# Optimization experiments

Hardware: AMD Instinct MI355X
Metric: run time of the kernel (lower is better)

## Reference

```python
import jax, jax.numpy as jnp
import numpy as np

H = 512

def setup_inputs() -> dict:
    key = jax.random.key(0)
    ks = jax.random.split(key, 10)
    T, B, S = 64, 8, 512
    scale = 1.0 / np.sqrt(H)
    return {
        "attn_dec_state": jax.random.normal(ks[0], (T, B, H), jnp.float32),
        "attn_enc_state": jax.random.normal(ks[1], (S, B, H), jnp.float32),
        "attn_coverage": jax.random.uniform(ks[2], (B, S), jnp.float32),
        "Wq": jax.random.normal(ks[3], (H, H), jnp.float32) * scale,   # linear_query weight (in,out)
        "bq": jnp.zeros((H,), jnp.float32),
        "Wc": jax.random.normal(ks[4], (H, H), jnp.float32) * scale,   # linear_context weight
        "v": jax.random.normal(ks[5], (H,), jnp.float32) * scale,       # v projection H->1
        "Wo": jax.random.normal(ks[6], (2 * H, H), jnp.float32) * scale,  # linear_out weight
        "bo": jnp.zeros((H,), jnp.float32),
        "wcov": jax.random.normal(ks[7], (H,), jnp.float32) * scale,    # linear_cover weight 1->H
    }

def reference(attn_dec_state, attn_enc_state, attn_coverage, Wq, bq, Wc, v, Wo, bo, wcov):
    dec = jnp.transpose(attn_dec_state, (1, 0, 2))   # [B,T,H]
    enc = jnp.transpose(attn_enc_state, (1, 0, 2))   # [B,S,H]
    # coverage: linear_cover(1->H) applied to each scalar, added to enc, then tanh
    enc = jnp.tanh(enc + attn_coverage[:, :, None] * wcov)  # [B,S,H]
    # additive (Bahdanau) score with broadcast-tanh
    a1 = jnp.einsum('bth,hk->btk', dec, Wq) + bq             # [B,T,H]
    a2 = jnp.einsum('bsh,hk->bsk', enc, Wc)                  # [B,S,H]
    scores = jnp.einsum('btsh,h->bts', jnp.tanh(a1[:, :, None, :] + a2[:, None, :, :]), v)  # [B,T,S]
    align = jax.nn.softmax(scores, axis=-1)                  # [B,T,S]
    c = jnp.einsum('bts,bsh->bth', align, enc)               # [B,T,H]
    concat = jnp.concatenate([c, dec], axis=-1)              # [B,T,2H]
    attn_h = jnp.einsum('btd,dk->btk', concat, Wo) + bo      # [B,T,H]
    attn_h = jnp.transpose(attn_h, (1, 0, 2))                # [T,B,H]
    align_out = jnp.transpose(align, (1, 0, 2))              # [T,B,S]
    return attn_h, align_out
```

## Files before the change

### kernel.cpp

```cpp
#include <hip/hip_runtime.h>
#include <cstddef>

static constexpr int TT = 64;
static constexpr int BB = 8;
static constexpr int SS = 512;
static constexpr int HH = 512;

typedef __attribute__((ext_vector_type(8))) short bf16x8;
typedef __attribute__((ext_vector_type(4))) float f32x4;

__device__ __forceinline__ float fast_tanh(float x) {
  float e = __expf(2.0f * x);
  return 1.0f - 2.0f * __builtin_amdgcn_rcpf(e + 1.0f);
}
__device__ __forceinline__ unsigned short f2bf(float f) {
  unsigned u = __float_as_uint(f);
  return (unsigned short)((u + 0x7FFFu + ((u >> 16) & 1u)) >> 16);
}

__global__ __launch_bounds__(256)
void k_prep(const float* __restrict__ enc, const float* __restrict__ cov,
            const float* __restrict__ wcov, const float* __restrict__ dec,
            const float* __restrict__ Wq, const float* __restrict__ Wc,
            const float* __restrict__ Wo,
            unsigned short* __restrict__ encpb, unsigned short* __restrict__ concatb,
            unsigned short* __restrict__ WqT, unsigned short* __restrict__ WcT,
            unsigned short* __restrict__ WoT) {
  __shared__ float tile[32][33];
  const int blk = blockIdx.x, tid = threadIdx.x;

  if (blk < 8192) {
    const int idx = blk * 256 + tid;
    const int h = idx & 511;
    const int bs = idx >> 9;
    const int s = bs & 511, b = bs >> 9;
    const float x = enc[(size_t)(s * BB + b) * HH + h] + cov[bs] * wcov[h];
    encpb[idx] = f2bf(fast_tanh(x));
  } else if (blk < 8704) {
    const int m = blk - 8192, t = m & 63, b = m >> 6;
    const float2 dv = *(const float2*)(dec + (size_t)(t * BB + b) * HH + 2 * tid);
    ((unsigned*)concatb)[(size_t)m * 512 + 256 + tid] =
        (unsigned)f2bf(dv.x) | ((unsigned)f2bf(dv.y) << 16);
  } else {
    int l = blk - 8704;
    const float* W; unsigned short* WT; int KT;
    if (l < 256)      { W = Wq; WT = WqT; KT = 512; }
    else if (l < 512) { W = Wc; WT = WcT; KT = 512; l -= 256; }
    else              { W = Wo; WT = WoT; KT = 1024; l -= 512; }
    const int n0 = (l & 15) * 32, k0 = (l >> 4) * 32;
    const int r = tid >> 3, c4 = (tid & 7) * 4;
    const float4 w = *(const float4*)(W + (size_t)(k0 + r) * 512 + n0 + c4);
    tile[r][c4 + 0] = w.x; tile[r][c4 + 1] = w.y;
    tile[r][c4 + 2] = w.z; tile[r][c4 + 3] = w.w;
    __syncthreads();
    unsigned short* o = WT + (size_t)(n0 + r) * KT + k0 + c4;
#pragma unroll
    for (int i = 0; i < 4; ++i) o[i] = f2bf(tile[c4 + i][r]);
  }
}

template<int LDA, int LDB>
__device__ __forceinline__ void gemm_tile(const unsigned short* __restrict__ A,
                                          const unsigned short* __restrict__ BT,
                                          int m0, int n0, int kbeg, int kend,
                                          unsigned short (*As)[72],
                                          unsigned short (*Bs)[72],
                                          f32x4 acc[4]) {
  const int tid = threadIdx.x, w = tid >> 6, lane = tid & 63;
  const int lr = tid >> 2, lk = (tid & 3) * 16;
  const int fm = w * 16 + (lane & 15), fk = (lane >> 4) * 8;
  for (int k0 = kbeg; k0 < kend; k0 += 64) {
    const uint4* ga = (const uint4*)(A + (size_t)(m0 + lr) * LDA + k0 + lk);
    const uint4* gb = (const uint4*)(BT + (size_t)(n0 + lr) * LDB + k0 + lk);
    uint4 a0 = ga[0], a1 = ga[1], b0 = gb[0], b1 = gb[1];
    *(uint4*)&As[lr][lk] = a0;  *(uint4*)&As[lr][lk + 8] = a1;
    *(uint4*)&Bs[lr][lk] = b0;  *(uint4*)&Bs[lr][lk + 8] = b1;
    __syncthreads();
#pragma unroll
    for (int ks = 0; ks < 2; ++ks) {
      bf16x8 af = *(const bf16x8*)&As[fm][ks * 32 + fk];
#pragma unroll
      for (int j = 0; j < 4; ++j) {
        bf16x8 bf = *(const bf16x8*)&Bs[j * 16 + (lane & 15)][ks * 32 + fk];
        acc[j] = __builtin_amdgcn_mfma_f32_16x16x32_bf16(af, bf, acc[j], 0, 0, 0);
      }
    }
    __syncthreads();
  }
}

__global__ __launch_bounds__(256)
void k_gemm12(const unsigned short* __restrict__ concatb,
              const unsigned short* __restrict__ encpb,
              const unsigned short* __restrict__ WqT,
              const unsigned short* __restrict__ WcT,
              const unsigned short* __restrict__ WoT,
              const float* __restrict__ bq, const float* __restrict__ bo,
              float* __restrict__ Ea1, float* __restrict__ Ea2,
              float* __restrict__ attn_h) {
  __shared__ unsigned short As[64][72];
  __shared__ unsigned short Bs[64][72];
  const int g = blockIdx.x, tid = threadIdx.x;
  const int w = tid >> 6, lane = tid & 63;
  const int col = lane & 15, rq = lane >> 4;

  if (g < 64) {
    const int m0 = (g >> 3) * 64, n0 = (g & 7) * 64;
    f32x4 acc[4] = {};
    gemm_tile<1024, 512>(concatb + 512, WqT, m0, n0, 0, 512, As, Bs, acc);
#pragma unroll
    for (int j = 0; j < 4; ++j) {
      const int n = n0 + j * 16 + col;
      const float bv = bq[n];
#pragma unroll
      for (int r = 0; r < 4; ++r) {
        const int m = m0 + w * 16 + rq * 4 + r;
        float val = fminf(fmaxf(acc[j][r] + bv, -30.0f), 30.0f);
        Ea1[(size_t)m * 512 + n] = __expf(2.0f * val);
      }
    }
  } else if (g < 576) {
    const int u = g - 64;
    const int m0 = (u >> 3) * 64, n0 = (u & 7) * 64;
    f32x4 acc[4] = {};
    gemm_tile<512, 512>(encpb, WcT, m0, n0, 0, 512, As, Bs, acc);
#pragma unroll
    for (int j = 0; j < 4; ++j) {
      const int n = n0 + j * 16 + col;
#pragma unroll
      for (int r = 0; r < 4; ++r) {
        const int m = m0 + w * 16 + rq * 4 + r;
        float val = fminf(fmaxf(acc[j][r], -30.0f), 30.0f);
        Ea2[(size_t)m * 512 + n] = __expf(2.0f * val);
      }
    }
  } else {
    const int u = g - 576;
    const int m0 = (u >> 3) * 64, n0 = (u & 7) * 64;
    f32x4 acc[4] = {};
    gemm_tile<1024, 1024>(concatb, WoT, m0, n0, 512, 1024, As, Bs, acc);
#pragma unroll
    for (int j = 0; j < 4; ++j) {
      const int n = n0 + j * 16 + col;
      const float bv = bo[n];
#pragma unroll
      for (int r = 0; r < 4; ++r) {
        const int m = m0 + w * 16 + rq * 4 + r;
        const int bi = m >> 6, t = m & 63;
        attn_h[(size_t)(t * BB + bi) * 512 + n] = acc[j][r] + bv;
      }
    }
  }
}

__global__ __launch_bounds__(512)
void k_attn(const float* __restrict__ Ea1, const float* __restrict__ Ea2,
            const float* __restrict__ v, const unsigned short* __restrict__ encpb,
            float* __restrict__ align_out, unsigned short* __restrict__ concatb) {
  __shared__ __align__(16) char smem[12352];
  float (*sc)[512]   = (float(*)[512])smem;
  float (*ea1s)[512] = (float(*)[512])(smem + 4096);
  float* v2s         = (float*)(smem + 8192);
  float2* part       = (float2*)(smem + 4096);
  float (*red)[8]    = (float(*)[8])(smem + 12288);

  const int g = blockIdx.x, tid = threadIdx.x;
  const int b = g & 7, t0 = (g >> 3) * 2;
  const int wv = tid >> 6, lane = tid & 63;
  const int hq = lane & 3, sl = lane >> 2;

  ea1s[0][tid] = Ea1[(size_t)(b * TT + t0) * HH + tid];
  ea1s[1][tid] = Ea1[(size_t)(b * TT + t0 + 1) * HH + tid];
  v2s[tid] = 2.0f * v[tid];
  __syncthreads();

#define TERM(E1, E2, VV, A) A = fmaf(VV, __builtin_amdgcn_rcpf(fmaf(E1, E2, 1.0f)), A)
  for (int p = 0; p < 2; ++p) {
    const int s0 = p * 256 + wv * 32 + sl;
    const float* e2p0 = Ea2 + (size_t)(b * SS + s0) * HH;
    const float* e2p1 = e2p0 + (size_t)16 * HH;
    float acc[2][2] = {};
#pragma unroll 4
    for (int it = 0; it < 32; ++it) {
      const int h = it * 16 + hq * 4;
      const float4 e20 = *(const float4*)(e2p0 + h);
      const float4 e21 = *(const float4*)(e2p1 + h);
      const float4 vvv = *(const float4*)&v2s[h];
      float4 e1r[2];
      e1r[0] = *(const float4*)&ea1s[0][h];
      e1r[1] = *(const float4*)&ea1s[1][h];
#pragma unroll
      for (int i = 0; i < 2; ++i) {
        TERM(e1r[i].x, e20.x, vvv.x, acc[i][0]);
        TERM(e1r[i].y, e20.y, vvv.y, acc[i][0]);
        TERM(e1r[i].z, e20.z, vvv.z, acc[i][0]);
        TERM(e1r[i].w, e20.w, vvv.w, acc[i][0]);
        TERM(e1r[i].x, e21.x, vvv.x, acc[i][1]);
        TERM(e1r[i].y, e21.y, vvv.y, acc[i][1]);
        TERM(e1r[i].z, e21.z, vvv.z, acc[i][1]);
        TERM(e1r[i].w, e21.w, vvv.w, acc[i][1]);
      }
    }
#pragma unroll
    for (int i = 0; i < 2; ++i)
#pragma unroll
      for (int j = 0; j < 2; ++j) {
        acc[i][j] += __shfl_xor(acc[i][j], 1);
        acc[i][j] += __shfl_xor(acc[i][j], 2);
      }
    if (hq == 0) {
      sc[0][s0] = -acc[0][0]; sc[0][s0 + 16] = -acc[0][1];
      sc[1][s0] = -acc[1][0]; sc[1][s0 + 16] = -acc[1][1];
    }
  }
#undef TERM
  __syncthreads();

  const float x0 = sc[0][tid], x1 = sc[1][tid];
  float m0 = x0, m1 = x1;
#pragma unroll
  for (int off = 32; off; off >>= 1) {
    m0 = fmaxf(m0, __shfl_xor(m0, off));
    m1 = fmaxf(m1, __shfl_xor(m1, off));
  }
  if (lane == 0) { red[0][wv] = m0; red[1][wv] = m1; }
  __syncthreads();
  m0 = red[0][0]; m1 = red[1][0];
#pragma unroll
  for (int w2 = 1; w2 < 8; ++w2) { m0 = fmaxf(m0, red[0][w2]); m1 = fmaxf(m1, red[1][w2]); }
  __syncthreads();
  const float e0 = __expf(x0 - m0), e1 = __expf(x1 - m1);
  float s0v = e0, s1v = e1;
#pragma unroll
  for (int off = 32; off; off >>= 1) {
    s0v += __shfl_xor(s0v, off);
    s1v += __shfl_xor(s1v, off);
  }
  if (lane == 0) { red[0][wv] = s0v; red[1][wv] = s1v; }
  __syncthreads();
  float sum0 = 0.f, sum1 = 0.f;
#pragma unroll
  for (int w2 = 0; w2 < 8; ++w2) { sum0 += red[0][w2]; sum1 += red[1][w2]; }
  const float a0 = e0 * __builtin_amdgcn_rcpf(sum0);
  const float a1 = e1 * __builtin_amdgcn_rcpf(sum1);

  align_out[(size_t)(t0 + 0) * BB * SS + b * SS + tid] = a0;
  align_out[(size_t)(t0 + 1) * BB * SS + b * SS + tid] = a1;
  sc[0][tid] = a0;
  sc[1][tid] = a1;
  __syncthreads();

  {
    const int sh = tid >> 8, hp = tid & 255;
    const unsigned* ep = (const unsigned*)encpb + (size_t)b * SS * 256;
    float c00 = 0.f, c01 = 0.f, c10 = 0.f, c11 = 0.f;
#pragma unroll 8
    for (int s2 = sh * 256; s2 < sh * 256 + 256; ++s2) {
      const unsigned u = ep[s2 * 256 + hp];
      const float elo = __uint_as_float(u << 16);
      const float ehi = __uint_as_float(u & 0xffff0000u);
      const float av0 = sc[0][s2], av1 = sc[1][s2];
      c00 = fmaf(av0, elo, c00); c01 = fmaf(av0, ehi, c01);
      c10 = fmaf(av1, elo, c10); c11 = fmaf(av1, ehi, c11);
    }
    part[(0 * 2 + sh) * 256 + hp] = make_float2(c00, c01);
    part[(1 * 2 + sh) * 256 + hp] = make_float2(c10, c11);
  }
  __syncthreads();
  {
    const int t = tid >> 8, hp = tid & 255;
    const float2 pa = part[(t * 2 + 0) * 256 + hp];
    const float2 pb = part[(t * 2 + 1) * 256 + hp];
    const float clo = pa.x + pb.x, chi = pa.y + pb.y;
    ((unsigned*)concatb)[(size_t)(b * TT + t0 + t) * 512 + hp] =
        (unsigned)f2bf(clo) | ((unsigned)f2bf(chi) << 16);
  }
}

__global__ __launch_bounds__(256)
void k_out(const unsigned short* __restrict__ A,
           const unsigned short* __restrict__ BT,
           float* __restrict__ C) {
  __shared__ unsigned short As[64][72];
  __shared__ unsigned short Bs[64][72];
  const int tid = threadIdx.x;
  const int w = tid >> 6, lane = tid & 63;
  const int tau = blockIdx.x >> 2, kc = blockIdx.x & 3;
  const int n0 = (tau & 7) * 64, m0 = (tau >> 3) * 64;

  f32x4 acc[4] = {};
  gemm_tile<1024, 1024>(A, BT, m0, n0, kc * 128, kc * 128 + 128, As, Bs, acc);

  const int col = lane & 15, rq = lane >> 4;
#pragma unroll
  for (int j = 0; j < 4; ++j) {
    const int n = n0 + j * 16 + col;
#pragma unroll
    for (int r = 0; r < 4; ++r) {
      const int m = m0 + w * 16 + rq * 4 + r;
      const int bi = m >> 6, t = m & 63;
      unsafeAtomicAdd(&C[(size_t)(t * BB + bi) * 512 + n], acc[j][r]);
    }
  }
}

extern "C" void kernel_launch(void* const* d_in, const int* in_sizes, int n_in,
                              void* d_out, int out_size, void* d_ws, size_t ws_size,
                              hipStream_t stream) {
  const float* dec  = (const float*)d_in[0];
  const float* enc  = (const float*)d_in[1];
  const float* cov  = (const float*)d_in[2];
  const float* Wq   = (const float*)d_in[3];
  const float* bq   = (const float*)d_in[4];
  const float* Wc   = (const float*)d_in[5];
  const float* v    = (const float*)d_in[6];
  const float* Wo   = (const float*)d_in[7];
  const float* bo   = (const float*)d_in[8];
  const float* wcov = (const float*)d_in[9];

  float* out = (float*)d_out;
  float* attn_h    = out;
  float* align_out = out + (size_t)TT * BB * HH;

  char* w = (char*)d_ws;
  const size_t MB = 1024 * 1024;
  unsigned short* encpb   = (unsigned short*)(w);
  unsigned short* WqT     = (unsigned short*)(w + 4 * MB);
  unsigned short* WcT     = (unsigned short*)(w + 4 * MB + 512 * 1024);
  unsigned short* WoT     = (unsigned short*)(w + 5 * MB);
  unsigned short* concatb = (unsigned short*)(w + 6 * MB);
  float*          Ea1     = (float*)(w + 7 * MB);
  float*          Ea2     = (float*)(w + 8 * MB);

  k_prep<<<9728, 256, 0, stream>>>(enc, cov, wcov, dec, Wq, Wc, Wo,
                                   encpb, concatb, WqT, WcT, WoT);
  k_gemm12<<<640, 256, 0, stream>>>(concatb, encpb, WqT, WcT, WoT, bq, bo,
                                    Ea1, Ea2, attn_h);
  k_attn<<<256, 512, 0, stream>>>(Ea1, Ea2, v, encpb, align_out, concatb);
  k_out<<<256, 256, 0, stream>>>(concatb, WoT, attn_h);
}
```

Before: 132.9 us.

## Fuse context-half output projection into attention kernel and vectorize prep

The separate k_out kernel, which ran a split-K GEMM of the context half of concat against Wo with atomic adds, is removed. Its work now happens inside k_attn: each block converts its two context rows to bf16 in shared memory and multiplies them against WoT with MFMA, adding the result to attn_h directly. The prep kernel also now handles four elements per thread with float4 loads and ushort4 stores, which cuts the block count. This saves one kernel launch and the concatb round trip, but the fused MFMA pads M from 2 rows to 16 and reads WoT from global memory in every block without shared-memory reuse.

```diff
diff --git a/kernel.cpp b/kernel.cpp
--- a/kernel.cpp
+++ b/kernel.cpp
@@ -29,20 +29,28 @@
   __shared__ float tile[32][33];
   const int blk = blockIdx.x, tid = threadIdx.x;
 
-  if (blk < 8192) {
-    const int idx = blk * 256 + tid;
-    const int h = idx & 511;
-    const int bs = idx >> 9;
+  if (blk < 2048) {
+    const int r = tid >> 7, c = (tid & 127) * 4;
+    const int bs = blk * 2 + r;
     const int s = bs & 511, b = bs >> 9;
-    const float x = enc[(size_t)(s * BB + b) * HH + h] + cov[bs] * wcov[h];
-    encpb[idx] = f2bf(fast_tanh(x));
-  } else if (blk < 8704) {
-    const int m = blk - 8192, t = m & 63, b = m >> 6;
-    const float2 dv = *(const float2*)(dec + (size_t)(t * BB + b) * HH + 2 * tid);
-    ((unsigned*)concatb)[(size_t)m * 512 + 256 + tid] =
-        (unsigned)f2bf(dv.x) | ((unsigned)f2bf(dv.y) << 16);
+    const float4 ev = *(const float4*)(enc + (size_t)(s * BB + b) * HH + c);
+    const float cv = cov[bs];
+    const float4 wv = *(const float4*)(wcov + c);
+    ushort4 o;
+    o.x = f2bf(fast_tanh(ev.x + cv * wv.x));
+    o.y = f2bf(fast_tanh(ev.y + cv * wv.y));
+    o.z = f2bf(fast_tanh(ev.z + cv * wv.z));
+    o.w = f2bf(fast_tanh(ev.w + cv * wv.w));
+    *(ushort4*)(encpb + (size_t)bs * HH + c) = o;
+  } else if (blk < 2304) {
+    const int r = tid >> 7, c = (tid & 127) * 4;
+    const int m = (blk - 2048) * 2 + r, t = m & 63, b = m >> 6;
+    const float4 dv = *(const float4*)(dec + (size_t)(t * BB + b) * HH + c);
+    ushort4 o;
+    o.x = f2bf(dv.x); o.y = f2bf(dv.y); o.z = f2bf(dv.z); o.w = f2bf(dv.w);
+    *(ushort4*)(concatb + (size_t)m * 1024 + 512 + c) = o;
   } else {
-    int l = blk - 8704;
+    int l = blk - 2304;
     const float* W; unsigned short* WT; int KT;
     if (l < 256)      { W = Wq; WT = WqT; KT = 512; }
     else if (l < 512) { W = Wc; WT = WcT; KT = 512; l -= 256; }
@@ -156,13 +164,15 @@
 __global__ __launch_bounds__(512)
 void k_attn(const float* __restrict__ Ea1, const float* __restrict__ Ea2,
             const float* __restrict__ v, const unsigned short* __restrict__ encpb,
-            float* __restrict__ align_out, unsigned short* __restrict__ concatb) {
-  __shared__ __align__(16) char smem[12352];
+            const unsigned short* __restrict__ WoT,
+            float* __restrict__ align_out, float* __restrict__ attn_h) {
+  __shared__ __align__(16) char smem[14400];
   float (*sc)[512]   = (float(*)[512])smem;
   float (*ea1s)[512] = (float(*)[512])(smem + 4096);
   float* v2s         = (float*)(smem + 8192);
   float2* part       = (float2*)(smem + 4096);
-  float (*red)[8]    = (float(*)[8])(smem + 12288);
+  unsigned short* c2b = (unsigned short*)(smem + 12288);
+  float (*red)[8]    = (float(*)[8])(smem + 14336);
 
   const int g = blockIdx.x, tid = threadIdx.x;
   const int b = g & 7, t0 = (g >> 3) * 2;
@@ -271,35 +281,35 @@
     const int t = tid >> 8, hp = tid & 255;
     const float2 pa = part[(t * 2 + 0) * 256 + hp];
     const float2 pb = part[(t * 2 + 1) * 256 + hp];
-    const float clo = pa.x + pb.x, chi = pa.y + pb.y;
-    ((unsigned*)concatb)[(size_t)(b * TT + t0 + t) * 512 + hp] =
-        (unsigned)f2bf(clo) | ((unsigned)f2bf(chi) << 16);
-  }
-}
-
-__global__ __launch_bounds__(256)
-void k_out(const unsigned short* __restrict__ A,
-           const unsigned short* __restrict__ BT,
-           float* __restrict__ C) {
-  __shared__ unsigned short As[64][72];
-  __shared__ unsigned short Bs[64][72];
-  const int tid = threadIdx.x;
-  const int w = tid >> 6, lane = tid & 63;
-  const int tau = blockIdx.x >> 2, kc = blockIdx.x & 3;
-  const int n0 = (tau & 7) * 64, m0 = (tau >> 3) * 64;
-
-  f32x4 acc[4] = {};
-  gemm_tile<1024, 1024>(A, BT, m0, n0, kc * 128, kc * 128 + 128, As, Bs, acc);
-
-  const int col = lane & 15, rq = lane >> 4;
-#pragma unroll
-  for (int j = 0; j < 4; ++j) {
-    const int n = n0 + j * 16 + col;
-#pragma unroll
-    for (int r = 0; r < 4; ++r) {
-      const int m = m0 + w * 16 + rq * 4 + r;
-      const int bi = m >> 6, t = m & 63;
-      unsafeAtomicAdd(&C[(size_t)(t * BB + bi) * 512 + n], acc[j][r]);
+    ((unsigned*)c2b)[t * 256 + hp] =
+        (unsigned)f2bf(pa.x + pb.x) | ((unsigned)f2bf(pa.y + pb.y) << 16);
+  }
+  __syncthreads();
+
+  {
+    const int n0 = wv * 64;
+    const int fm = lane & 15, fko = (lane >> 4) * 8;
+    f32x4 acc[4] = {};
+    for (int k0 = 0; k0 < 512; k0 += 32) {
+      bf16x8 af = {};
+      if (fm < 2) af = *(const bf16x8*)&c2b[fm * 512 + k0 + fko];
+#pragma unroll
+      for (int j = 0; j < 4; ++j) {
+        const bf16x8 bf = *(const bf16x8*)(WoT +
+            (size_t)(n0 + j * 16 + fm) * 1024 + k0 + fko);
+        acc[j] = __builtin_amdgcn_mfma_f32_16x16x32_bf16(af, bf, acc[j], 0, 0, 0);
+      }
+    }
+    if (lane < 16) {
+#pragma unroll
+      for (int j = 0; j < 4; ++j) {
+        const int n = n0 + j * 16 + lane;
+#pragma unroll
+        for (int r = 0; r < 2; ++r) {
+          float* p = attn_h + (size_t)((t0 + r) * BB + b) * 512 + n;
+          *p += acc[j][r];
+        }
+      }
     }
   }
 }
@@ -332,10 +342,9 @@
   float*          Ea1     = (float*)(w + 7 * MB);
   float*          Ea2     = (float*)(w + 8 * MB);
 
-  k_prep<<<9728, 256, 0, stream>>>(enc, cov, wcov, dec, Wq, Wc, Wo,
+  k_prep<<<3328, 256, 0, stream>>>(enc, cov, wcov, dec, Wq, Wc, Wo,
                                    encpb, concatb, WqT, WcT, WoT);
   k_gemm12<<<640, 256, 0, stream>>>(concatb, encpb, WqT, WcT, WoT, bq, bo,
                                     Ea1, Ea2, attn_h);
-  k_attn<<<256, 512, 0, stream>>>(Ea1, Ea2, v, encpb, align_out, concatb);
-  k_out<<<256, 256, 0, stream>>>(concatb, WoT, attn_h);
-}
+  k_attn<<<256, 512, 0, stream>>>(Ea1, Ea2, v, encpb, WoT, align_out, attn_h);
+}
```

Result: slower. 141.7 us (+6.6%).
